# Kernel tuning notes

Hardware: AMD Instinct MI355X
Metric: run time of the kernel (lower is better)

Reference implementation:

```python
import jax, jax.numpy as jnp
import numpy as np

BINS = 256
VMIN = 0.0
VMAX = 1.0
SIGMA = 30.0
DELTA = (VMAX - VMIN) / BINS


def setup_inputs() -> dict:
    key = jax.random.key(0)
    y = jax.random.uniform(key, (4, 1, 512, 512), dtype=jnp.float32)
    return {"y": y}


def reference(y) -> jnp.ndarray:
    b, _, h, w = y.shape
    yf = y.reshape(b, 1, -1)                      # (b, 1, h*w)
    centers = VMIN + DELTA * (jnp.arange(BINS, dtype=jnp.float32) + 0.5)
    c = centers.reshape(1, BINS, 1)               # (1, bins, 1)
    x = yf - c                                    # (b, bins, h*w) broadcast
    k = jax.nn.sigmoid(SIGMA * (x + DELTA / 2)) - jax.nn.sigmoid(SIGMA * (x - DELTA / 2))
    hist = jnp.sum(k, axis=2)                     # (b, bins)
    p = hist / (h * w) + 1e-6
    d = jnp.sum(-p * jnp.log(p))
    return 1.0 / d
```

## Files before the change

kernel.cpp:

```cpp
#include <hip/hip_runtime.h>
#include <math.h>

#define NB 4
#define BINS 256
#define HW (512*512)

#define CHUNKS 64
#define PIX_PER_BLOCK (HW / CHUNKS)
#define F4_PER_THREAD (PIX_PER_BLOCK / 4 / 256)


__global__ __launch_bounds__(256) void hist_part(const float* __restrict__ y,
                                                 unsigned* __restrict__ Hp,
                                                 float* __restrict__ acc) {
    __shared__ unsigned lh[BINS];
    const int t = threadIdx.x;
    lh[t] = 0u;
    if (blockIdx.x == 0 && blockIdx.y == 0 && t == 0) {
        acc[0] = 0.0f;
        ((unsigned*)acc)[1] = 0u;
    }
    __syncthreads();

    const int b = blockIdx.y;
    const float4* src = reinterpret_cast<const float4*>(
        y + (size_t)b * HW + (size_t)blockIdx.x * PIX_PER_BLOCK);

#pragma unroll
    for (int i = 0; i < F4_PER_THREAD; ++i) {
        float4 v = src[t + 256 * i];
        float vals[4] = {v.x, v.y, v.z, v.w};
#pragma unroll
        for (int c = 0; c < 4; ++c) {
            int bin = (int)(vals[c] * 256.0f);
            bin = bin < 0 ? 0 : (bin > 255 ? 255 : bin);
            atomicAdd(&lh[bin], 1u);
        }
    }
    __syncthreads();
    Hp[((size_t)b * CHUNKS + blockIdx.x) * BINS + t] = lh[t];
}

__global__ __launch_bounds__(256) void entropy_fused(const unsigned* __restrict__ Hp,
                                                     float* __restrict__ acc,
                                                     float* __restrict__ out) {
    __shared__ float K0[512];
    __shared__ float Hs[BINS];
    __shared__ float red[4];

    const int t = threadIdx.x;
    const int b = blockIdx.x;
    const float DELTA = 1.0f / 256.0f;
    const float SIGMA = 30.0f;

    unsigned H = 0u;
    const unsigned* hb = Hp + (size_t)b * CHUNKS * BINS + t;
#pragma unroll 8
    for (int c = 0; c < CHUNKS; ++c) H += hb[c * BINS];
    Hs[t] = (float)H;

    for (int i = t; i < 2 * BINS - 1; i += 256) {
        float x = (float)(i - (BINS - 1)) * DELTA;
        float sp = 1.0f / (1.0f + __expf(-SIGMA * (x + 0.5f * DELTA)));
        float sm = 1.0f / (1.0f + __expf(-SIGMA * (x - 0.5f * DELTA)));
        K0[i] = sp - sm;
    }
    __syncthreads();

    const int j = t;
    float hist = 0.0f;
#pragma unroll 8
    for (int m = 0; m < BINS; ++m) {
        hist = fmaf(Hs[m], K0[m - j + (BINS - 1)], hist);
    }

    float p = hist * (1.0f / (float)HW) + 1e-6f;
    float e = -p * __logf(p);

    const int lane = t & 63, wid = t >> 6;
#pragma unroll
    for (int off = 32; off > 0; off >>= 1) e += __shfl_down(e, off);
    if (lane == 0) red[wid] = e;
    __syncthreads();

    if (t == 0) {
        float part = red[0] + red[1] + red[2] + red[3];
        atomicAdd(acc, part);
        __threadfence();
        unsigned old = atomicAdd(((unsigned*)acc) + 1, 1u);
        if (old == NB - 1) {
            __threadfence();
            float d = atomicAdd(acc, 0.0f);
            out[0] = 1.0f / d;
        }
    }
}

extern "C" void kernel_launch(void* const* d_in, const int* in_sizes, int n_in,
                              void* d_out, int out_size, void* d_ws, size_t ws_size,
                              hipStream_t stream) {
    const float* y = (const float*)d_in[0];
    unsigned* Hp = (unsigned*)d_ws;
    float* acc = (float*)(Hp + NB * CHUNKS * BINS);

    hist_part<<<dim3(CHUNKS, NB), 256, 0, stream>>>(y, Hp, acc);
    entropy_fused<<<NB, 256, 0, stream>>>(Hp, acc, (float*)d_out);
}
```

Baseline: 61.13 us.

## Fuse histogram and entropy kernels with last-block-done reduction

Merges the two launches into one kernel of 1024-thread blocks. Each block bins one float4 per thread, and the last block per batch, found through an atomic counter, reduces the partial histograms and computes the entropy. The smoothing convolution is restricted to a band of taps, computed incrementally from adjacent sigmoids and split across four thread groups. A memset is added to reset the control counters, and the banded kernel truncates tails that the full convolution included.

```diff
diff --git a/kernel.cpp b/kernel.cpp
--- a/kernel.cpp
+++ b/kernel.cpp
@@ -7,28 +7,37 @@
 
 #define CHUNKS 64
 #define PIX_PER_BLOCK (HW / CHUNKS)
-#define F4_PER_THREAD (PIX_PER_BLOCK / 4 / 256)
+#define HIST_BLOCKS (NB * CHUNKS)
+#define THREADS 1024
+
+#define M_LO 64
+#define GTAPS 32
+#define HSP (M_LO + BINS + 64)
 
 
-__global__ __launch_bounds__(256) void hist_part(const float* __restrict__ y,
-                                                 unsigned* __restrict__ Hp,
-                                                 float* __restrict__ acc) {
+__global__ __launch_bounds__(THREADS) void fused_entropy(
+        const float* __restrict__ y,
+        unsigned* __restrict__ Hp,
+        unsigned* __restrict__ ctrl,
+        float* __restrict__ out) {
     __shared__ unsigned lh[BINS];
+    __shared__ float Hs4[4][BINS];
+    __shared__ float Hs_pad[HSP];
+    __shared__ float red[4];
+    __shared__ unsigned amLast;
+
     const int t = threadIdx.x;
-    lh[t] = 0u;
-    if (blockIdx.x == 0 && blockIdx.y == 0 && t == 0) {
-        acc[0] = 0.0f;
-        ((unsigned*)acc)[1] = 0u;
-    }
+    const int bid = blockIdx.x;
+    const int b = bid >> 6;
+    const int chunk = bid & 63;
+
+    if (t < BINS) lh[t] = 0u;
     __syncthreads();
 
-    const int b = blockIdx.y;
     const float4* src = reinterpret_cast<const float4*>(
-        y + (size_t)b * HW + (size_t)blockIdx.x * PIX_PER_BLOCK);
-
-#pragma unroll
-    for (int i = 0; i < F4_PER_THREAD; ++i) {
-        float4 v = src[t + 256 * i];
+        y + (size_t)b * HW + (size_t)chunk * PIX_PER_BLOCK);
+    float4 v = src[t];
+    {
         float vals[4] = {v.x, v.y, v.z, v.w};
 #pragma unroll
         for (int c = 0; c < 4; ++c) {
@@ -38,59 +47,74 @@
         }
     }
     __syncthreads();
-    Hp[((size_t)b * CHUNKS + blockIdx.x) * BINS + t] = lh[t];
-}
+    if (t < BINS) Hp[(size_t)bid * BINS + t] = lh[t];
+    __syncthreads();
 
-__global__ __launch_bounds__(256) void entropy_fused(const unsigned* __restrict__ Hp,
-                                                     float* __restrict__ acc,
-                                                     float* __restrict__ out) {
-    __shared__ float K0[512];
-    __shared__ float Hs[BINS];
-    __shared__ float red[4];
+    if (t == 0) {
+        __threadfence();
+        unsigned old = __hip_atomic_fetch_add(&ctrl[b], 1u,
+                        __ATOMIC_ACQ_REL, __HIP_MEMORY_SCOPE_AGENT);
+        amLast = (old == CHUNKS - 1) ? 1u : 0u;
+    }
+    __syncthreads();
+    if (!amLast) return;
+    __threadfence();
 
-    const int t = threadIdx.x;
-    const int b = blockIdx.x;
-    const float DELTA = 1.0f / 256.0f;
-    const float SIGMA = 30.0f;
+    const int bin = t & 255;
+    const int g = t >> 8;
 
-    unsigned H = 0u;
-    const unsigned* hb = Hp + (size_t)b * CHUNKS * BINS + t;
-#pragma unroll 8
-    for (int c = 0; c < CHUNKS; ++c) H += hb[c * BINS];
-    Hs[t] = (float)H;
+    float H = 0.0f;
+    const unsigned* hb = Hp + ((size_t)(b * CHUNKS + g * 16) * BINS) + bin;
+#pragma unroll
+    for (int c = 0; c < 16; ++c) H += (float)hb[(size_t)c * BINS];
+    Hs4[g][bin] = H;
+    __syncthreads();
 
-    for (int i = t; i < 2 * BINS - 1; i += 256) {
-        float x = (float)(i - (BINS - 1)) * DELTA;
-        float sp = 1.0f / (1.0f + __expf(-SIGMA * (x + 0.5f * DELTA)));
-        float sm = 1.0f / (1.0f + __expf(-SIGMA * (x - 0.5f * DELTA)));
-        K0[i] = sp - sm;
+    if (t < HSP) {
+        float hv = 0.0f;
+        int j = t - M_LO;
+        if (j >= 0 && j < BINS)
+            hv = Hs4[0][j] + Hs4[1][j] + Hs4[2][j] + Hs4[3][j];
+        Hs_pad[t] = hv;
     }
     __syncthreads();
 
-    const int j = t;
-    float hist = 0.0f;
-#pragma unroll 8
-    for (int m = 0; m < BINS; ++m) {
-        hist = fmaf(Hs[m], K0[m - j + (BINS - 1)], hist);
+    const float DELTA = 1.0f / 256.0f;
+    const float SIGMA = 30.0f;
+    const float base = (float)(g * GTAPS - M_LO) * DELTA;
+    float acc = 0.0f;
+    float s_prev = 1.0f / (1.0f + __expf(-SIGMA * (base - 0.5f * DELTA)));
+    const float* hp = &Hs_pad[bin + g * GTAPS];
+#pragma unroll
+    for (int i = 0; i < GTAPS; ++i) {
+        float s_next = 1.0f / (1.0f + __expf(-SIGMA * (base + ((float)i + 0.5f) * DELTA)));
+        acc = fmaf(s_next - s_prev, hp[i], acc);
+        s_prev = s_next;
     }
+    __syncthreads();
+    Hs4[g][bin] = acc;
+    __syncthreads();
 
-    float p = hist * (1.0f / (float)HW) + 1e-6f;
-    float e = -p * __logf(p);
-
-    const int lane = t & 63, wid = t >> 6;
+    float e = 0.0f;
+    if (t < BINS) {
+        float hist = Hs4[0][t] + Hs4[1][t] + Hs4[2][t] + Hs4[3][t];
+        float p = hist * (1.0f / (float)HW) + 1e-6f;
+        e = -p * __logf(p);
+    }
 #pragma unroll
     for (int off = 32; off > 0; off >>= 1) e += __shfl_down(e, off);
-    if (lane == 0) red[wid] = e;
+    if (t < BINS && (t & 63) == 0) red[t >> 6] = e;
     __syncthreads();
 
     if (t == 0) {
         float part = red[0] + red[1] + red[2] + red[3];
-        atomicAdd(acc, part);
+        atomicAdd((float*)&ctrl[5], part);
         __threadfence();
-        unsigned old = atomicAdd(((unsigned*)acc) + 1, 1u);
+        unsigned old = __hip_atomic_fetch_add(&ctrl[4], 1u,
+                        __ATOMIC_ACQ_REL, __HIP_MEMORY_SCOPE_AGENT);
         if (old == NB - 1) {
-            __threadfence();
-            float d = atomicAdd(acc, 0.0f);
+            float d = __hip_atomic_load((float*)&ctrl[5],
+                        __ATOMIC_ACQUIRE, __HIP_MEMORY_SCOPE_AGENT);
             out[0] = 1.0f / d;
         }
     }
@@ -100,9 +124,9 @@
                               void* d_out, int out_size, void* d_ws, size_t ws_size,
                               hipStream_t stream) {
     const float* y = (const float*)d_in[0];
-    unsigned* Hp = (unsigned*)d_ws;
-    float* acc = (float*)(Hp + NB * CHUNKS * BINS);
+    unsigned* ctrl = (unsigned*)d_ws;
+    unsigned* Hp = ctrl + 64;
 
-    hist_part<<<dim3(CHUNKS, NB), 256, 0, stream>>>(y, Hp, acc);
-    entropy_fused<<<NB, 256, 0, stream>>>(Hp, acc, (float*)d_out);
+    hipMemsetAsync(d_ws, 0, 64 * sizeof(unsigned), stream);
+    fused_entropy<<<HIST_BLOCKS, THREADS, 0, stream>>>(y, Hp, ctrl, (float*)d_out);
 }
```

After: 75.77 us. +24.0%, slower.
